# Performance work log

Hardware: AMD Instinct MI355X
Metric: run time of the kernel (lower is better)

Reference implementation:

```python
import jax, jax.numpy as jnp
import numpy as np

DIM = 1024
N = 8192


def setup_inputs() -> dict:
    key = jax.random.key(0)
    k_x, k_w, k_b = jax.random.split(key, 3)
    inputs = jax.random.normal(k_x, (N, DIM), dtype=jnp.float32)
    # nn.Bilinear(dimension, dimension, 1): weight shape (1, d, d), bias shape (1,)
    bound = 1.0 / np.sqrt(DIM)
    W = jax.random.uniform(k_w, (DIM, DIM), jnp.float32, -bound, bound)
    b = jax.random.uniform(k_b, (1,), jnp.float32, -bound, bound)
    return {"inputs": inputs, "W": W, "b": b}


def reference(inputs, W, b):
    # out[i, j] = inputs[i] @ W @ inputs[j] + b  ==  (X @ W) @ X^T + b
    # Algebraically identical to repeat+nn.Bilinear, without the N^2*d blowup.
    xw = inputs @ W              # (N, d)
    out = xw @ inputs.T + b[0]   # (N, N)
    return out
```

## Files before the change

kernel.cpp:

```cpp
#include <hip/hip_runtime.h>
#include <hip/hip_bf16.h>

typedef __bf16 bf16;
typedef __bf16 bf16x8 __attribute__((ext_vector_type(8)));
typedef __bf16 bf16x4 __attribute__((ext_vector_type(4)));
typedef float  f32x4  __attribute__((ext_vector_type(4)));

#define GLD_LDS(g, l)                                                        \
  __builtin_amdgcn_global_load_lds(                                          \
      (const __attribute__((address_space(1))) void*)(g),                    \
      (__attribute__((address_space(3))) void*)(l), 16, 0, 0)

#define SB()    __builtin_amdgcn_s_barrier()
#define LG0()   asm volatile("s_waitcnt lgkmcnt(0)" ::: "memory")
#define WVM2()  asm volatile("s_waitcnt vmcnt(2)" ::: "memory")
#define WVM0()  asm volatile("s_waitcnt vmcnt(0)" ::: "memory")
#define PRIO1() __builtin_amdgcn_s_setprio(1)
#define PRIO0() __builtin_amdgcn_s_setprio(0)

__global__ __launch_bounds__(512, 2)
void gemm256(const bf16* __restrict__ A, const bf16* __restrict__ B,
             float* __restrict__ C, const float* __restrict__ bias_p,
             int M, int N, int K) {
  extern __shared__ bf16 lds[];
  const int tid  = threadIdx.x;
  const int lane = tid & 63, wave = tid >> 6;
  const int wm = wave >> 2, wn = wave & 3;
  const int fr = lane & 15, fq = lane >> 4;
  const int xm = (fr & 7) << 4;
  const int kx0 = (fq * 16) ^ xm;
  const int kx1 = (fq * 16 + 64) ^ xm;

  const int nwg = gridDim.x;
  const int bid = blockIdx.x;
  const int swz = (bid & 7) * (nwg >> 3) + (bid >> 3);
  const int gx  = N >> 8;
  const int row0 = (swz / gx) << 8, col0 = (swz % gx) << 8;

  const int srow = wave * 8 + (lane >> 3);
  const int scol = ((lane & 7) ^ (lane >> 3)) * 8;
  const bf16* Agl = A + (size_t)(row0 + srow) * K + scol;
  const bf16* Bgl = B + (size_t)(col0 + srow) * K + scol;

#define STG(gl, tb, t, h)                                                    \
  do {                                                                       \
    const size_t _k = (size_t)(t) * 64;                                      \
    GLD_LDS((gl) + (size_t)((h) * 128) * K + _k,                             \
            lds + (tb) + ((t) & 1) * 16384 + (h) * 8192 + wave * 512);       \
    GLD_LDS((gl) + (size_t)((h) * 128 + 64) * K + _k,                        \
            lds + (tb) + ((t) & 1) * 16384 + (h) * 8192 + 4096 + wave * 512);\
  } while (0)

  const char* ldsc = (const char*)lds;
  const char* Ab0 = ldsc + wm * 16384 + fr * 128 + kx0;
  const char* Ab1 = ldsc + wm * 16384 + fr * 128 + kx1;
  const char* Bb0 = ldsc + 65536 + wn * 8192 + fr * 128 + kx0;
  const char* Bb1 = ldsc + 65536 + wn * 8192 + fr * 128 + kx1;

  f32x4  acc[8][4] = {};
  bf16x8 af[4][2];
  bf16x8 bg[4][2];

#define LDA(mg, p)                                                           \
  do {                                                                       \
    _Pragma("unroll") for (int m_ = 0; m_ < 4; ++m_) {                       \
      af[m_][0] = *(const bf16x8*)(Ab0 + (p) * 32768 + ((mg) * 4 + m_) * 2048);\
      af[m_][1] = *(const bf16x8*)(Ab1 + (p) * 32768 + ((mg) * 4 + m_) * 2048);\
    }                                                                        \
  } while (0)

#define LDB(np, p)                                                           \
  do {                                                                       \
    _Pragma("unroll") for (int n_ = 0; n_ < 2; ++n_) {                       \
      bg[(np) * 2 + n_][0] =                                                 \
          *(const bf16x8*)(Bb0 + (p) * 32768 + ((np) * 2 + n_) * 2048);      \
      bg[(np) * 2 + n_][1] =                                                 \
          *(const bf16x8*)(Bb1 + (p) * 32768 + ((np) * 2 + n_) * 2048);      \
    }                                                                        \
  } while (0)

#define MM(mg, np)                                                           \
  do {                                                                       \
    _Pragma("unroll") for (int kk_ = 0; kk_ < 2; ++kk_)                      \
      _Pragma("unroll") for (int m_ = 0; m_ < 4; ++m_)                       \
        _Pragma("unroll") for (int n_ = 0; n_ < 2; ++n_)                     \
          acc[(mg) * 4 + m_][(np) * 2 + n_] =                                \
              __builtin_amdgcn_mfma_f32_16x16x32_bf16(                       \
                  af[m_][kk_], bg[(np) * 2 + n_][kk_],                       \
                  acc[(mg) * 4 + m_][(np) * 2 + n_], 0, 0, 0);               \
  } while (0)

  STG(Agl, 0, 0, 0); STG(Agl, 0, 0, 1);
  STG(Bgl, 32768, 0, 0); STG(Bgl, 32768, 0, 1);
  STG(Agl, 0, 1, 0);
  WVM2(); SB();

  const int NT = K >> 6;
  for (int T = 0; T < NT; T += 2) {
    const bool s2 = (T + 2 < NT), s3 = (T + 3 < NT);
    LDA(0, 0); LDB(0, 0);
    STG(Agl, 0, T + 1, 1);
    SB(); LG0(); PRIO1(); MM(0, 0); PRIO0(); SB();
    LDB(1, 0);
    STG(Bgl, 32768, T + 1, 0);
    SB(); LG0(); PRIO1(); MM(0, 1); PRIO0(); SB();
    LDA(1, 0);
    STG(Bgl, 32768, T + 1, 1);
    SB(); LG0(); PRIO1(); MM(1, 0); PRIO0(); SB();
    if (s2) STG(Agl, 0, T + 2, 0);
    SB(); PRIO1(); MM(1, 1); PRIO0();
    if (s2) { WVM2(); } else { WVM0(); }
    SB();
    LDA(0, 1); LDB(0, 1);
    if (s2) STG(Agl, 0, T + 2, 1);
    SB(); LG0(); PRIO1(); MM(0, 0); PRIO0(); SB();
    LDB(1, 1);
    if (s2) STG(Bgl, 32768, T + 2, 0);
    SB(); LG0(); PRIO1(); MM(0, 1); PRIO0(); SB();
    LDA(1, 1);
    if (s2) STG(Bgl, 32768, T + 2, 1);
    SB(); LG0(); PRIO1(); MM(1, 0); PRIO0(); SB();
    if (s3) STG(Agl, 0, T + 3, 0);
    SB(); PRIO1(); MM(1, 1); PRIO0();
    if (s3) { WVM2(); } else { WVM0(); }
    SB();
  }

  const float bias = bias_p[0];
#pragma unroll
  for (int m = 0; m < 8; ++m) {
#pragma unroll
    for (int n = 0; n < 4; ++n) {
      const int r = row0 + wm * 128 + m * 16 + fq * 4;
      const int c = col0 + wn * 64 + n * 16 + fr;
#pragma unroll
      for (int j = 0; j < 4; ++j)
        C[(size_t)(r + j) * N + c] = acc[m][n][j] + bias;
    }
  }
#undef STG
#undef LDA
#undef LDB
#undef MM
}

__global__ void gemm_bt(const bf16* __restrict__ A, const bf16* __restrict__ B,
                        bf16* __restrict__ Cb, int M, int N, int K) {
  __shared__ bf16 As[128 * 32];
  __shared__ bf16 Bs[128 * 32];
  const int tid  = threadIdx.x;
  const int lane = tid & 63;
  const int wave = tid >> 6;
  const int wr = wave >> 1, wc = wave & 1;
  const int fr = lane & 15, fq = lane >> 4;
  const int row0 = blockIdx.y * 128, col0 = blockIdx.x * 128;

  f32x4 acc[4][4] = {};
  const int c0 = tid, c1 = 256 + tid;
  const bf16* Ag0 = A + (size_t)(row0 + (c0 >> 2)) * K + (c0 & 3) * 8;
  const bf16* Ag1 = A + (size_t)(row0 + (c1 >> 2)) * K + (c1 & 3) * 8;
  const bf16* Bg0 = B + (size_t)(col0 + (c0 >> 2)) * K + (c0 & 3) * 8;
  const bf16* Bg1 = B + (size_t)(col0 + (c1 >> 2)) * K + (c1 & 3) * 8;
  bf16* Al0 = As + (wave * 64) * 8;
  bf16* Al1 = As + (256 + wave * 64) * 8;
  bf16* Bl0 = Bs + (wave * 64) * 8;
  bf16* Bl1 = Bs + (256 + wave * 64) * 8;

  for (int k0 = 0; k0 < K; k0 += 32) {
    GLD_LDS(Ag0 + k0, Al0);
    GLD_LDS(Ag1 + k0, Al1);
    GLD_LDS(Bg0 + k0, Bl0);
    GLD_LDS(Bg1 + k0, Bl1);
    __syncthreads();
    bf16x8 af[4], bgf[4];
#pragma unroll
    for (int m = 0; m < 4; ++m)
      af[m] = *(const bf16x8*)&As[(wr * 64 + m * 16 + fr) * 32 + fq * 8];
#pragma unroll
    for (int n = 0; n < 4; ++n)
      bgf[n] = *(const bf16x8*)&Bs[(wc * 64 + n * 16 + fr) * 32 + fq * 8];
#pragma unroll
    for (int m = 0; m < 4; ++m)
#pragma unroll
      for (int n = 0; n < 4; ++n)
        acc[m][n] = __builtin_amdgcn_mfma_f32_16x16x32_bf16(af[m], bgf[n],
                                                            acc[m][n], 0, 0, 0);
    __syncthreads();
  }
#pragma unroll
  for (int m = 0; m < 4; ++m)
#pragma unroll
    for (int n = 0; n < 4; ++n) {
      const int r  = row0 + wr * 64 + m * 16 + fq * 4;
      const int cc = col0 + wc * 64 + n * 16 + fr;
#pragma unroll
      for (int j = 0; j < 4; ++j)
        Cb[(size_t)(r + j) * N + cc] = (bf16)acc[m][n][j];
    }
}

__global__ void cvt_f32_bf16(const float* __restrict__ in, bf16* __restrict__ out,
                             int n4) {
  int i = blockIdx.x * blockDim.x + threadIdx.x;
  if (i >= n4) return;
  const float4 v = ((const float4*)in)[i];
  bf16x4 o;
  o[0] = (bf16)v.x; o[1] = (bf16)v.y; o[2] = (bf16)v.z; o[3] = (bf16)v.w;
  ((bf16x4*)out)[i] = o;
}

__global__ void transpose_cvt_w(const float* __restrict__ W, bf16* __restrict__ Wt) {
  __shared__ float s[32][33];
  const int tx = threadIdx.x & 31;
  const int ty = threadIdx.x >> 5;
  const int n0 = blockIdx.x * 32;
  const int k0 = blockIdx.y * 32;
#pragma unroll
  for (int p = 0; p < 4; ++p)
    s[ty + p * 8][tx] = W[(size_t)(k0 + ty + p * 8) * 1024 + n0 + tx];
  __syncthreads();
#pragma unroll
  for (int p = 0; p < 4; ++p)
    Wt[(size_t)(n0 + ty + p * 8) * 1024 + k0 + tx] = (bf16)s[tx][ty + p * 8];
}

extern "C" void kernel_launch(void* const* d_in, const int* in_sizes, int n_in,
                              void* d_out, int out_size, void* d_ws, size_t ws_size,
                              hipStream_t stream) {
  const float* X = (const float*)d_in[0];
  const float* W = (const float*)d_in[1];
  const float* b = (const float*)d_in[2];
  float* out = (float*)d_out;

  const int Nn = 8192, D = 1024;
  char* ws = (char*)d_ws;
  bf16* Xb  = (bf16*)(ws);
  bf16* XWb = (bf16*)(ws + (size_t)16 * 1024 * 1024);
  bf16* Wt  = (bf16*)(ws + (size_t)32 * 1024 * 1024);

  cvt_f32_bf16<<<(Nn * D / 4 + 255) / 256, 256, 0, stream>>>(X, Xb, Nn * D / 4);
  transpose_cvt_w<<<dim3(D / 32, D / 32), 256, 0, stream>>>(W, Wt);
  gemm_bt<<<dim3(D / 128, Nn / 128), 256, 0, stream>>>(Xb, Wt, XWb, Nn, D, D);
  gemm256<<<(Nn / 256) * (Nn / 256), 512, 131072, stream>>>(XWb, Xb, out, b,
                                                            Nn, Nn, D);
}
```

Baseline: 198.0 us.

## Double-buffer MFMA fragment registers and reschedule LDS/global prefetch in 256-tile GEMM

Splits the A and B register fragments into two sets (afA/afB, bgA/bgB) so LDS reads for the next MFMA group can be issued while the current group runs. It also prefetches a full second K-tile in the prologue and reshuffles where global-to-LDS stages and vmcnt waits sit inside the 8-phase loop. The goal is to hide LDS read latency and cut stall points between MFMA bursts. The cost is more VGPR pressure, which could hurt occupancy under the 512x2 launch bounds, and a more fragile wait-count schedule.

```diff
diff --git a/kernel.cpp b/kernel.cpp
--- a/kernel.cpp
+++ b/kernel.cpp
@@ -13,8 +13,7 @@
 
 #define SB()    __builtin_amdgcn_s_barrier()
 #define LG0()   asm volatile("s_waitcnt lgkmcnt(0)" ::: "memory")
-#define WVM2()  asm volatile("s_waitcnt vmcnt(2)" ::: "memory")
-#define WVM0()  asm volatile("s_waitcnt vmcnt(0)" ::: "memory")
+#define WVM(n)  asm volatile("s_waitcnt vmcnt(" #n ")" ::: "memory")
 #define PRIO1() __builtin_amdgcn_s_setprio(1)
 #define PRIO0() __builtin_amdgcn_s_setprio(0)
 
@@ -58,72 +57,69 @@
   const char* Bb1 = ldsc + 65536 + wn * 8192 + fr * 128 + kx1;
 
   f32x4  acc[8][4] = {};
-  bf16x8 af[4][2];
-  bf16x8 bg[4][2];
-
-#define LDA(mg, p)                                                           \
+  bf16x8 afA[4][2], afB[4][2];
+  bf16x8 bgA[2][2], bgB[2][2];
+
+#define LDAF(AF, mgo, p)                                                     \
   do {                                                                       \
     _Pragma("unroll") for (int m_ = 0; m_ < 4; ++m_) {                       \
-      af[m_][0] = *(const bf16x8*)(Ab0 + (p) * 32768 + ((mg) * 4 + m_) * 2048);\
-      af[m_][1] = *(const bf16x8*)(Ab1 + (p) * 32768 + ((mg) * 4 + m_) * 2048);\
+      AF[m_][0] = *(const bf16x8*)(Ab0 + (p) * 32768 + (mgo) + m_ * 2048);   \
+      AF[m_][1] = *(const bf16x8*)(Ab1 + (p) * 32768 + (mgo) + m_ * 2048);   \
     }                                                                        \
   } while (0)
 
-#define LDB(np, p)                                                           \
+#define LDBF(BG, npo, p)                                                     \
   do {                                                                       \
     _Pragma("unroll") for (int n_ = 0; n_ < 2; ++n_) {                       \
-      bg[(np) * 2 + n_][0] =                                                 \
-          *(const bf16x8*)(Bb0 + (p) * 32768 + ((np) * 2 + n_) * 2048);      \
-      bg[(np) * 2 + n_][1] =                                                 \
-          *(const bf16x8*)(Bb1 + (p) * 32768 + ((np) * 2 + n_) * 2048);      \
+      BG[n_][0] = *(const bf16x8*)(Bb0 + (p) * 32768 + (npo) + n_ * 2048);   \
+      BG[n_][1] = *(const bf16x8*)(Bb1 + (p) * 32768 + (npo) + n_ * 2048);   \
     }                                                                        \
   } while (0)
 
-#define MM(mg, np)                                                           \
+#define MMX(AF, BG, mg, np)                                                  \
   do {                                                                       \
     _Pragma("unroll") for (int kk_ = 0; kk_ < 2; ++kk_)                      \
       _Pragma("unroll") for (int m_ = 0; m_ < 4; ++m_)                       \
         _Pragma("unroll") for (int n_ = 0; n_ < 2; ++n_)                     \
           acc[(mg) * 4 + m_][(np) * 2 + n_] =                                \
               __builtin_amdgcn_mfma_f32_16x16x32_bf16(                       \
-                  af[m_][kk_], bg[(np) * 2 + n_][kk_],                       \
+                  AF[m_][kk_], BG[n_][kk_],                                  \
                   acc[(mg) * 4 + m_][(np) * 2 + n_], 0, 0, 0);               \
   } while (0)
 
   STG(Agl, 0, 0, 0); STG(Agl, 0, 0, 1);
   STG(Bgl, 32768, 0, 0); STG(Bgl, 32768, 0, 1);
-  STG(Agl, 0, 1, 0);
-  WVM2(); SB();
+  STG(Agl, 0, 1, 0); STG(Agl, 0, 1, 1);
+  STG(Bgl, 32768, 1, 0); STG(Bgl, 32768, 1, 1);
+  WVM(8); SB();
+  LDAF(afA, 0, 0); LDBF(bgA, 0, 0);
 
   const int NT = K >> 6;
   for (int T = 0; T < NT; T += 2) {
-    const bool s2 = (T + 2 < NT), s3 = (T + 3 < NT);
-    LDA(0, 0); LDB(0, 0);
-    STG(Agl, 0, T + 1, 1);
-    SB(); LG0(); PRIO1(); MM(0, 0); PRIO0(); SB();
-    LDB(1, 0);
-    STG(Bgl, 32768, T + 1, 0);
-    SB(); LG0(); PRIO1(); MM(0, 1); PRIO0(); SB();
-    LDA(1, 0);
-    STG(Bgl, 32768, T + 1, 1);
-    SB(); LG0(); PRIO1(); MM(1, 0); PRIO0(); SB();
-    if (s2) STG(Agl, 0, T + 2, 0);
-    SB(); PRIO1(); MM(1, 1); PRIO0();
-    if (s2) { WVM2(); } else { WVM0(); }
+    const bool s2 = (T + 2 < NT);
+    LDBF(bgB, 4096, 0);
+    SB(); LG0(); PRIO1(); MMX(afA, bgA, 0, 0); PRIO0(); SB();
+    LDAF(afB, 8192, 0);
+    if (s2) STG(Bgl, 32768, T + 2, 0);
+    SB(); LG0(); PRIO1(); MMX(afA, bgB, 0, 1); PRIO0(); SB();
+    if (s2) STG(Bgl, 32768, T + 2, 1);
+    SB(); PRIO1(); MMX(afB, bgA, 1, 0); PRIO0();
+    if (s2) { WVM(4); } else { WVM(0); }
     SB();
-    LDA(0, 1); LDB(0, 1);
-    if (s2) STG(Agl, 0, T + 2, 1);
-    SB(); LG0(); PRIO1(); MM(0, 0); PRIO0(); SB();
-    LDB(1, 1);
-    if (s2) STG(Bgl, 32768, T + 2, 0);
-    SB(); LG0(); PRIO1(); MM(0, 1); PRIO0(); SB();
-    LDA(1, 1);
-    if (s2) STG(Bgl, 32768, T + 2, 1);
-    SB(); LG0(); PRIO1(); MM(1, 0); PRIO0(); SB();
-    if (s3) STG(Agl, 0, T + 3, 0);
-    SB(); PRIO1(); MM(1, 1); PRIO0();
-    if (s3) { WVM2(); } else { WVM0(); }
+    LDAF(afA, 0, 1); LDBF(bgA, 0, 1);
+    if (s2) { STG(Agl, 0, T + 2, 0); STG(Agl, 0, T + 2, 1); }
+    SB(); PRIO1(); MMX(afB, bgB, 1, 1); PRIO0(); SB();
+    LDBF(bgB, 4096, 1);
+    SB(); LG0(); PRIO1(); MMX(afA, bgA, 0, 0); PRIO0(); SB();
+    LDAF(afB, 8192, 1);
+    if (s2) STG(Bgl, 32768, T + 3, 0);
+    SB(); LG0(); PRIO1(); MMX(afA, bgB, 0, 1); PRIO0(); SB();
+    if (s2) { STG(Bgl, 32768, T + 3, 1); STG(Agl, 0, T + 3, 0); STG(Agl, 0, T + 3, 1); }
+    SB(); PRIO1(); MMX(afB, bgA, 1, 0); PRIO0();
+    if (s2) { WVM(8); } else { WVM(0); }
     SB();
+    if (s2) { LDAF(afA, 0, 0); LDBF(bgA, 0, 0); }
+    SB(); PRIO1(); MMX(afB, bgB, 1, 1); PRIO0(); SB();
   }
 
   const float bias = bias_p[0];
@@ -139,9 +135,9 @@
     }
   }
 #undef STG
-#undef LDA
-#undef LDB
-#undef MM
+#undef LDAF
+#undef LDBF
+#undef MMX
 }
 
 __global__ void gemm_bt(const bf16* __restrict__ A, const bf16* __restrict__ B,
```

Result: slower. 255.1 us (+28.8%).

## Reuse tuned 256-tile GEMM for X@W and remap tiles for L2 locality

Applied to the files above, without the earlier changes.

Replaces the simple 128x128 first-stage GEMM with the pipelined 256x256 kernel, templated to emit either bf16 without bias or fp32 with bias. For the large 8192x8192 GEMM, it adds a tile mapping that groups each XCD's blocks into 4x8 tile patches per round, aiming for better L2 reuse of A and B panels. The first GEMM now launches only 128 workgroups of 512 threads, which may underfill the device, but it is a small share of the total work.

```diff
diff --git a/kernel.cpp b/kernel.cpp
--- a/kernel.cpp
+++ b/kernel.cpp
@@ -18,10 +18,11 @@
 #define PRIO1() __builtin_amdgcn_s_setprio(1)
 #define PRIO0() __builtin_amdgcn_s_setprio(0)
 
+template <int EPI>
 __global__ __launch_bounds__(512, 2)
 void gemm256(const bf16* __restrict__ A, const bf16* __restrict__ B,
-             float* __restrict__ C, const float* __restrict__ bias_p,
-             int M, int N, int K) {
+             bf16* __restrict__ Cb, float* __restrict__ Cf,
+             const float* __restrict__ bias_p, int M, int N, int K) {
   extern __shared__ bf16 lds[];
   const int tid  = threadIdx.x;
   const int lane = tid & 63, wave = tid >> 6;
@@ -33,9 +34,18 @@
 
   const int nwg = gridDim.x;
   const int bid = blockIdx.x;
-  const int swz = (bid & 7) * (nwg >> 3) + (bid >> 3);
   const int gx  = N >> 8;
-  const int row0 = (swz / gx) << 8, col0 = (swz % gx) << 8;
+  int tile_r, tile_c;
+  if (gx == 32 && (M >> 8) == 32) {
+    const int round = bid >> 8, idx = bid & 255;
+    const int xcd = idx & 7, pos = idx >> 3;
+    tile_r = (round >> 1) * 16 + (xcd >> 1) * 4 + (pos >> 3);
+    tile_c = (round & 1) * 16 + (xcd & 1) * 8 + (pos & 7);
+  } else {
+    const int swz = (bid & 7) * (nwg >> 3) + (bid >> 3);
+    tile_r = swz / gx; tile_c = swz % gx;
+  }
+  const int row0 = tile_r << 8, col0 = tile_c << 8;
 
   const int srow = wave * 8 + (lane >> 3);
   const int scol = ((lane & 7) ^ (lane >> 3)) * 8;
@@ -126,7 +136,7 @@
     SB();
   }
 
-  const float bias = bias_p[0];
+  const float bias = (EPI == 1) ? bias_p[0] : 0.0f;
 #pragma unroll
   for (int m = 0; m < 8; ++m) {
 #pragma unroll
@@ -134,69 +144,18 @@
       const int r = row0 + wm * 128 + m * 16 + fq * 4;
       const int c = col0 + wn * 64 + n * 16 + fr;
 #pragma unroll
-      for (int j = 0; j < 4; ++j)
-        C[(size_t)(r + j) * N + c] = acc[m][n][j] + bias;
+      for (int j = 0; j < 4; ++j) {
+        if (EPI == 1)
+          Cf[(size_t)(r + j) * N + c] = acc[m][n][j] + bias;
+        else
+          Cb[(size_t)(r + j) * N + c] = (bf16)acc[m][n][j];
+      }
     }
   }
 #undef STG
 #undef LDA
 #undef LDB
 #undef MM
-}
-
-__global__ void gemm_bt(const bf16* __restrict__ A, const bf16* __restrict__ B,
-                        bf16* __restrict__ Cb, int M, int N, int K) {
-  __shared__ bf16 As[128 * 32];
-  __shared__ bf16 Bs[128 * 32];
-  const int tid  = threadIdx.x;
-  const int lane = tid & 63;
-  const int wave = tid >> 6;
-  const int wr = wave >> 1, wc = wave & 1;
-  const int fr = lane & 15, fq = lane >> 4;
-  const int row0 = blockIdx.y * 128, col0 = blockIdx.x * 128;
-
-  f32x4 acc[4][4] = {};
-  const int c0 = tid, c1 = 256 + tid;
-  const bf16* Ag0 = A + (size_t)(row0 + (c0 >> 2)) * K + (c0 & 3) * 8;
-  const bf16* Ag1 = A + (size_t)(row0 + (c1 >> 2)) * K + (c1 & 3) * 8;
-  const bf16* Bg0 = B + (size_t)(col0 + (c0 >> 2)) * K + (c0 & 3) * 8;
-  const bf16* Bg1 = B + (size_t)(col0 + (c1 >> 2)) * K + (c1 & 3) * 8;
-  bf16* Al0 = As + (wave * 64) * 8;
-  bf16* Al1 = As + (256 + wave * 64) * 8;
-  bf16* Bl0 = Bs + (wave * 64) * 8;
-  bf16* Bl1 = Bs + (256 + wave * 64) * 8;
-
-  for (int k0 = 0; k0 < K; k0 += 32) {
-    GLD_LDS(Ag0 + k0, Al0);
-    GLD_LDS(Ag1 + k0, Al1);
-    GLD_LDS(Bg0 + k0, Bl0);
-    GLD_LDS(Bg1 + k0, Bl1);
-    __syncthreads();
-    bf16x8 af[4], bgf[4];
-#pragma unroll
-    for (int m = 0; m < 4; ++m)
-      af[m] = *(const bf16x8*)&As[(wr * 64 + m * 16 + fr) * 32 + fq * 8];
-#pragma unroll
-    for (int n = 0; n < 4; ++n)
-      bgf[n] = *(const bf16x8*)&Bs[(wc * 64 + n * 16 + fr) * 32 + fq * 8];
-#pragma unroll
-    for (int m = 0; m < 4; ++m)
-#pragma unroll
-      for (int n = 0; n < 4; ++n)
-        acc[m][n] = __builtin_amdgcn_mfma_f32_16x16x32_bf16(af[m], bgf[n],
-                                                            acc[m][n], 0, 0, 0);
-    __syncthreads();
-  }
-#pragma unroll
-  for (int m = 0; m < 4; ++m)
-#pragma unroll
-    for (int n = 0; n < 4; ++n) {
-      const int r  = row0 + wr * 64 + m * 16 + fq * 4;
-      const int cc = col0 + wc * 64 + n * 16 + fr;
-#pragma unroll
-      for (int j = 0; j < 4; ++j)
-        Cb[(size_t)(r + j) * N + cc] = (bf16)acc[m][n][j];
-    }
 }
 
 __global__ void cvt_f32_bf16(const float* __restrict__ in, bf16* __restrict__ out,
@@ -240,7 +199,8 @@
 
   cvt_f32_bf16<<<(Nn * D / 4 + 255) / 256, 256, 0, stream>>>(X, Xb, Nn * D / 4);
   transpose_cvt_w<<<dim3(D / 32, D / 32), 256, 0, stream>>>(W, Wt);
-  gemm_bt<<<dim3(D / 128, Nn / 128), 256, 0, stream>>>(Xb, Wt, XWb, Nn, D, D);
-  gemm256<<<(Nn / 256) * (Nn / 256), 512, 131072, stream>>>(XWb, Xb, out, b,
-                                                            Nn, Nn, D);
-}
+  gemm256<0><<<(Nn / 256) * (D / 256), 512, 131072, stream>>>(
+      Xb, Wt, XWb, nullptr, nullptr, Nn, D, D);
+  gemm256<1><<<(Nn / 256) * (Nn / 256), 512, 131072, stream>>>(
+      XWb, Xb, nullptr, out, b, Nn, Nn, D);
+}
```

Measured after the change: 197.8 us. No clear change (-0.1%).
